# Kernel optimization log

Measured on AMD Instinct MI355X. Metric: run time of the kernel, lower is better.

Reference implementation:

```python
import jax, jax.numpy as jnp
import numpy as np

N_VIEWS = 4  # == view_size from init_kwargs
EPS = 1e-8


def setup_inputs() -> dict:
    key = jax.random.key(0)
    x = jax.random.normal(key, (32, 128, 32, 32), dtype=jnp.float32)  # [b*n, c, h, w]
    return {"x": x}


def reference(x):
    n = N_VIEWS
    bn, c, h, w = x.shape
    b = bn // n
    hw = h * w
    # per-pixel L2 normalization over channels (matches pow/sum/pow(0.5) + eps)
    norm = jnp.sqrt(jnp.sum(x * x, axis=1, keepdims=True))
    f = x / (norm + EPS)
    fn = f.reshape(b, n, c, hw)  # [b, n, c, hw]
    # off-diagonal view index table: for each reference view i, the n-1 other views j
    jj = np.array([[j for j in range(n) if j != i] for i in range(n)])  # [n, n-1]
    fA = fn[:, jj]  # [b, n, n-1, c, hw] -- view j features (A)
    # corr[b,i,k,p,q] = <view jj[i,k] at pixel p, view i at pixel q>
    # p indexes A pixels (channel dim of output), q indexes B (=view i) spatial pixels
    corr = jnp.einsum('bikcp,bicq->bikpq', fA, fn)  # [b, n, n-1, hw, hw]
    return corr.reshape(b * n * (n - 1), hw, h, w)
```

## Files before the change

### kernel.cpp

```cpp
#include <hip/hip_runtime.h>
#include <hip/hip_bf16.h>

typedef __attribute__((ext_vector_type(4))) float floatx4;
typedef __attribute__((ext_vector_type(8))) short shortx8;

#define HW   1024
#define C    128
#define EPS  1e-8f

__global__ __launch_bounds__(256) void norm_transpose(const float* __restrict__ x,
                                                      __hip_bfloat16* __restrict__ fnT) {
    int g = blockIdx.x * 256 + threadIdx.x;
    int v = g >> 10;
    int p = g & 1023;
    const float* xv = x + (size_t)v * (C * HW) + p;
    float s = 0.f;
#pragma unroll
    for (int c = 0; c < C; ++c) {
        float val = xv[(size_t)c * HW];
        s += val * val;
    }
    float scale = 1.0f / (sqrtf(s) + EPS);
    __hip_bfloat16* dst = fnT + (size_t)g * C;
#pragma unroll
    for (int c0 = 0; c0 < C; c0 += 8) {
        shortx8 pack;
#pragma unroll
        for (int u = 0; u < 8; ++u) {
            __hip_bfloat16 h = __float2bfloat16(xv[(size_t)(c0 + u) * HW] * scale);
            pack[u] = *(short*)&h;
        }
        *(shortx8*)(dst + c0) = pack;
    }
}

__global__ __launch_bounds__(256) void corr_gemm(const __hip_bfloat16* __restrict__ fnT,
                                                 float* __restrict__ out) {
    int g = blockIdx.z;
    int b = g / 12;
    int r = g % 12;
    int i = r / 3;
    int k = r % 3;
    int j = k + (k >= i);
    int vA = b * 4 + j;
    int vB = b * 4 + i;

    int lane = threadIdx.x & 63;
    int wave = threadIdx.x >> 6;
    int p0 = blockIdx.y * 128 + (wave >> 1) * 64;
    int q0 = blockIdx.x * 128 + (wave & 1) * 64;
    int lr   = lane & 15;
    int quad = lane >> 4;

    const __hip_bfloat16* Abase = fnT + (size_t)vA * (HW * C) + (size_t)(p0 + lr) * C + quad * 8;
    const __hip_bfloat16* Bbase = fnT + (size_t)vB * (HW * C) + (size_t)(q0 + lr) * C + quad * 8;

    floatx4 acc[4][4] = {};

#pragma unroll
    for (int kk = 0; kk < 4; ++kk) {
        int co = kk * 32;
        shortx8 a[4], bfr[4];
#pragma unroll
        for (int t = 0; t < 4; ++t) {
            a[t]   = *(const shortx8*)(Abase + (size_t)t * 16 * C + co);
            bfr[t] = *(const shortx8*)(Bbase + (size_t)t * 16 * C + co);
        }
#pragma unroll
        for (int mt = 0; mt < 4; ++mt)
#pragma unroll
            for (int nt = 0; nt < 4; ++nt)
                acc[mt][nt] = __builtin_amdgcn_mfma_f32_16x16x32_bf16(a[mt], bfr[nt], acc[mt][nt], 0, 0, 0);
    }

    float* outg = out + (size_t)g * HW * HW;
#pragma unroll
    for (int mt = 0; mt < 4; ++mt) {
#pragma unroll
        for (int rr = 0; rr < 4; ++rr) {
            int row = p0 + mt * 16 + quad * 4 + rr;
            float* orow = outg + (size_t)row * HW + q0 + lr;
#pragma unroll
            for (int nt = 0; nt < 4; ++nt)
                orow[nt * 16] = acc[mt][nt][rr];
        }
    }
}

extern "C" void kernel_launch(void* const* d_in, const int* in_sizes, int n_in,
                              void* d_out, int out_size, void* d_ws, size_t ws_size,
                              hipStream_t stream) {
    const float* x = (const float*)d_in[0];
    float* out = (float*)d_out;
    __hip_bfloat16* fnT = (__hip_bfloat16*)d_ws;

    norm_transpose<<<dim3(32 * 1024 / 256), 256, 0, stream>>>(x, fnT);
    corr_gemm<<<dim3(8, 8, 96), 256, 0, stream>>>(fnT, out);
}
```

Baseline: 448.8 us.

## Stage A/B tiles in LDS via direct global-to-LDS loads with XOR swizzle

```diff
diff --git a/kernel.cpp b/kernel.cpp
--- a/kernel.cpp
+++ b/kernel.cpp
@@ -34,8 +34,11 @@
     }
 }
 
-__global__ __launch_bounds__(256) void corr_gemm(const __hip_bfloat16* __restrict__ fnT,
-                                                 float* __restrict__ out) {
+__global__ __launch_bounds__(256, 2) void corr_gemm(const __hip_bfloat16* __restrict__ fnT,
+                                                    float* __restrict__ out) {
+    __shared__ __hip_bfloat16 Atile[128 * 128];
+    __shared__ __hip_bfloat16 Btile[128 * 128];
+
     int g = blockIdx.z;
     int b = g / 12;
     int r = g % 12;
@@ -47,24 +50,47 @@
 
     int lane = threadIdx.x & 63;
     int wave = threadIdx.x >> 6;
-    int p0 = blockIdx.y * 128 + (wave >> 1) * 64;
-    int q0 = blockIdx.x * 128 + (wave & 1) * 64;
+    int p0 = blockIdx.y * 128;
+    int q0 = blockIdx.x * 128;
+
+    const char* Ag = (const char*)(fnT + ((size_t)vA * HW + p0) * C);
+    const char* Bg = (const char*)(fnT + ((size_t)vB * HW + q0) * C);
+    char* Alds = (char*)&Atile[0];
+    char* Blds = (char*)&Btile[0];
+#pragma unroll
+    for (int t = 0; t < 8; ++t) {
+        int s = (wave * 8 + t) * 64 + lane;
+        int row = s >> 4;
+        int c16 = s & 15;
+        int goff = (row * 16 + (c16 ^ (row & 15))) * 16;
+        int loff = (wave * 8 + t) * 1024;
+        __builtin_amdgcn_global_load_lds(
+            (const __attribute__((address_space(1))) void*)(Ag + goff),
+            (__attribute__((address_space(3))) void*)(Alds + loff), 16, 0, 0);
+        __builtin_amdgcn_global_load_lds(
+            (const __attribute__((address_space(1))) void*)(Bg + goff),
+            (__attribute__((address_space(3))) void*)(Blds + loff), 16, 0, 0);
+    }
+    __syncthreads();
+
+    int wp = (wave >> 1) * 64;
+    int wq = (wave & 1) * 64;
     int lr   = lane & 15;
     int quad = lane >> 4;
 
-    const __hip_bfloat16* Abase = fnT + (size_t)vA * (HW * C) + (size_t)(p0 + lr) * C + quad * 8;
-    const __hip_bfloat16* Bbase = fnT + (size_t)vB * (HW * C) + (size_t)(q0 + lr) * C + quad * 8;
+    const char* Ab = (const char*)Atile + (size_t)(wp + lr) * 256;
+    const char* Bb = (const char*)Btile + (size_t)(wq + lr) * 256;
 
     floatx4 acc[4][4] = {};
 
 #pragma unroll
     for (int kk = 0; kk < 4; ++kk) {
-        int co = kk * 32;
+        int co = ((kk * 4 + quad) ^ lr) * 16;
         shortx8 a[4], bfr[4];
 #pragma unroll
         for (int t = 0; t < 4; ++t) {
-            a[t]   = *(const shortx8*)(Abase + (size_t)t * 16 * C + co);
-            bfr[t] = *(const shortx8*)(Bbase + (size_t)t * 16 * C + co);
+            a[t]   = *(const shortx8*)(Ab + t * 16 * 256 + co);
+            bfr[t] = *(const shortx8*)(Bb + t * 16 * 256 + co);
         }
 #pragma unroll
         for (int mt = 0; mt < 4; ++mt)
@@ -78,8 +104,8 @@
     for (int mt = 0; mt < 4; ++mt) {
 #pragma unroll
         for (int rr = 0; rr < 4; ++rr) {
-            int row = p0 + mt * 16 + quad * 4 + rr;
-            float* orow = outg + (size_t)row * HW + q0 + lr;
+            int row = p0 + wp + mt * 16 + quad * 4 + rr;
+            float* orow = outg + (size_t)row * HW + q0 + wq + lr;
 #pragma unroll
             for (int nt = 0; nt < 4; ++nt)
                 orow[nt * 16] = acc[mt][nt][rr];
```

Measured after the change: 410.3 us. 1.09x faster.
